# Kernel optimization log

Measured on AMD Instinct MI355X. Metric: run time of the kernel, lower is better.

## Reference

```python
import jax, jax.numpy as jnp
import numpy as np

NETWORK_STRIDE = 16
RPN_NMS_THRESHOLD = 0.7
N_OUT = 5  # top-N proposals returned ('N' in the source)
H = W = 32
NUM_ANCHORS = 9


def _conv(x, w, b, pad):
    y = jax.lax.conv_general_dilated(
        x, w, window_strides=(1, 1), padding=[(pad, pad), (pad, pad)],
        dimension_numbers=("NCHW", "OIHW", "NCHW"))
    return y + b[None, :, None, None]


def _construct_anchors(anchors_wh, h, w):
    # anchors_wh: [A,2] (already divided by NETWORK_STRIDE)
    base = jnp.concatenate([-anchors_wh / 2.0, anchors_wh / 2.0], axis=-1)  # [A,4]
    xs = jnp.arange(h, dtype=anchors_wh.dtype)
    ys = jnp.arange(w, dtype=anchors_wh.dtype)
    hf = jnp.asarray(h, anchors_wh.dtype)
    wf = jnp.asarray(w, anchors_wh.dtype)
    x1 = (base[None, None, :, 0] + xs[:, None, None]) / hf  # [h,1,A]
    y1 = (base[None, None, :, 1] + ys[None, :, None]) / wf  # [1,w,A]
    x2 = (base[None, None, :, 2] + xs[:, None, None]) / hf
    y2 = (base[None, None, :, 3] + ys[None, :, None]) / wf
    anc = jnp.stack(jnp.broadcast_arrays(x1, y1, x2, y2), axis=-1)  # [h,w,A,4]
    return anc.reshape(-1, 4)


def _deparameterize(reg, anchors):
    wa = anchors[:, 2] - anchors[:, 0]
    ha = anchors[:, 3] - anchors[:, 1]
    xa = (anchors[:, 0] + anchors[:, 2]) * 0.5
    ya = (anchors[:, 1] + anchors[:, 3]) * 0.5
    xc = reg[:, 0] * wa + xa
    yc = reg[:, 1] * ha + ya
    bw = jnp.exp(reg[:, 2]) * wa
    bh = jnp.exp(reg[:, 3]) * ha
    return jnp.stack([xc - bw / 2, yc - bh / 2, xc + bw / 2, yc + bh / 2], axis=-1)


def _pairwise_iou(a, b):
    lt = jnp.maximum(a[:, None, :2], b[None, :, :2])
    rb = jnp.minimum(a[:, None, 2:], b[None, :, 2:])
    wh = jnp.clip(rb - lt, 0.0)
    inter = wh[..., 0] * wh[..., 1]
    area_a = (a[:, 2] - a[:, 0]) * (a[:, 3] - a[:, 1])
    area_b = (b[:, 2] - b[:, 0]) * (b[:, 3] - b[:, 1])
    return inter / (area_a[:, None] + area_b[None, :] - inter)


def _nms(boxes, scores, thr):
    n = boxes.shape[0]
    order = jnp.argsort(-scores)
    boxes_s = boxes[order]
    iou = _pairwise_iou(boxes_s, boxes_s)  # [n,n], the memory-dominant intermediate
    idx = jnp.arange(n)

    def body(suppressed, i):
        keep_i = jnp.logical_not(suppressed[i])
        suppressed = suppressed | (keep_i & (iou[i] > thr) & (idx > i))
        return suppressed, keep_i

    _, kept = jax.lax.scan(body, jnp.zeros(n, dtype=bool), idx)
    # kept indices (in score order) first, padding slots pushed to the back
    sel = jnp.argsort(jnp.where(kept, idx, n))
    return order[sel]


def _forward(x, w_win, b_win, w_cls, b_cls, w_reg, b_reg, anchors_wh):
    feats = jax.nn.relu(_conv(x, w_win, b_win, 1))
    cls = _conv(feats, w_cls, b_cls, 0)
    reg = _conv(feats, w_reg, b_reg, 0)
    cls = jax.nn.softmax(cls.transpose(0, 2, 3, 1).reshape(-1, 2), axis=-1)
    reg = reg.transpose(0, 2, 3, 1).reshape(-1, 4)
    h, w = feats.shape[-2], feats.shape[-1]
    anchors = _construct_anchors(anchors_wh, h, w)
    boxes = _deparameterize(jax.lax.stop_gradient(reg), anchors)  # reg.detach()
    scores = cls[:, 0]
    keep = _nms(boxes, scores, RPN_NMS_THRESHOLD)[:N_OUT]
    return cls[keep], boxes[keep]


def setup_inputs() -> dict:
    key = jax.random.key(0)
    ks = jax.random.split(key, 4)
    anchors_px = np.array(
        [[184, 96], [128, 128], [88, 176], [368, 184], [256, 256],
         [176, 352], [736, 368], [512, 512], [352, 704]], dtype=np.float32)
    anchors_wh = jnp.asarray(anchors_px) / NETWORK_STRIDE
    x = jax.random.normal(ks[0], (1, 512, H, W), dtype=jnp.float32)
    w_win = jax.random.normal(ks[1], (512, 512, 3, 3), dtype=jnp.float32) * 0.02
    b_win = jnp.zeros((512,), jnp.float32)
    w_cls = jax.random.normal(ks[2], (2 * NUM_ANCHORS, 512, 1, 1), dtype=jnp.float32) * 0.02
    b_cls = jnp.zeros((2 * NUM_ANCHORS,), jnp.float32)
    w_reg = jax.random.normal(ks[3], (4 * NUM_ANCHORS, 512, 1, 1), dtype=jnp.float32) * 0.01
    b_reg = jnp.zeros((4 * NUM_ANCHORS,), jnp.float32)
    return {"x": x, "w_win": w_win, "b_win": b_win, "w_cls": w_cls,
            "b_cls": b_cls, "w_reg": w_reg, "b_reg": b_reg,
            "anchors_wh": anchors_wh}


def reference(x, w_win, b_win, w_cls, b_cls, w_reg, b_reg, anchors_wh):
    return _forward(x, w_win, b_win, w_cls, b_cls, w_reg, b_reg, anchors_wh)
```

## Files before the change

### kernel.cpp

```cpp
#include <hip/hip_runtime.h>
#include <math.h>


#define HH 32
#define WW 32
#define NPIX 1024
#define CIN 512
#define COUT 512
#define NA 9
#define NBOX (NPIX * NA)
#define NMS_THR 0.7f
#define NOUT 5

typedef _Float16 half8 __attribute__((ext_vector_type(8)));
typedef float f32x4 __attribute__((ext_vector_type(4)));

#define GLOAD16(src, dst) \
    __builtin_amdgcn_global_load_lds((const __attribute__((address_space(1))) void*)(src), \
                                     (__attribute__((address_space(3))) void*)(dst), 16, 0, 0)

__global__ __launch_bounds__(256) void prep_kernel(
    const float* __restrict__ x, const float* __restrict__ w,
    const float* __restrict__ w_cls, const float* __restrict__ b_cls,
    const float* __restrict__ w_reg, const float* __restrict__ b_reg,
    _Float16* __restrict__ xp_hi, _Float16* __restrict__ xp_lo,
    _Float16* __restrict__ wt_hi, _Float16* __restrict__ wt_lo,
    float* __restrict__ wt_head, float* __restrict__ bias_head)
{
    int b = blockIdx.x;
    int tid = threadIdx.x;
    if (b < 1024) {
        int t = b * 256 + tid;
#pragma unroll
        for (int q = 0; q < 9; ++q) {
            float v = w[(size_t)t * 9 + q];
            _Float16 hi = (_Float16)v;
            _Float16 lo = (_Float16)(v - (float)hi);
            wt_hi[(size_t)q * 262144 + t] = hi;
            wt_lo[(size_t)q * 262144 + t] = lo;
        }
    } else if (b < 1152) {
        __shared__ float xs[64][65];
        int bb = b - 1024;
        int ic0 = (bb & 7) * 64;
        int pix0 = (bb >> 3) * 64;
#pragma unroll
        for (int r = 0; r < 16; ++r) {
            int i = r * 4 + (tid >> 6);
            int j = tid & 63;
            xs[i][j] = x[(size_t)(ic0 + i) * NPIX + pix0 + j];
        }
        __syncthreads();
#pragma unroll
        for (int rr = 0; rr < 16; ++rr) {
            int j = rr * 4 + (tid >> 6);
            int i = tid & 63;
            float v = xs[i][j];
            int p = pix0 + j;
            int row = ((p >> 5) + 1) * 34 + (p & 31) + 1;
            _Float16 hi = (_Float16)v;
            _Float16 lo = (_Float16)(v - (float)hi);
            xp_hi[(size_t)row * 512 + ic0 + i] = hi;
            xp_lo[(size_t)row * 512 + ic0 + i] = lo;
        }
    } else if (b < 1188) {
        int base = (b - 1152) * 256 + tid;
        for (int e = base; e < 132 * 512; e += 36 * 256) {
            int br = e >> 9;
            int ic = e & 511;
            int row;
            if (br < 34) row = br;
            else if (br < 68) row = 33 * 34 + (br - 34);
            else { int c2 = br - 68; row = (1 + (c2 >> 1)) * 34 + (c2 & 1) * 33; }
            xp_hi[(size_t)row * 512 + ic] = (_Float16)0.f;
            xp_lo[(size_t)row * 512 + ic] = (_Float16)0.f;
        }
    } else {
        int t = (b - 1188) * 256 + tid;
        int o = t & 63;
        int ic0 = (t >> 6) * 16;
#pragma unroll
        for (int k = 0; k < 16; ++k) {
            int ic = ic0 + k;
            float v = 0.f;
            if (o < 18)      v = w_cls[(size_t)o * CIN + ic];
            else if (o < 54) v = w_reg[(size_t)(o - 18) * CIN + ic];
            wt_head[(size_t)ic * 64 + o] = v;
        }
        if (t < 64) {
            float bv = 0.f;
            if (t < 18)      bv = b_cls[t];
            else if (t < 54) bv = b_reg[t - 18];
            bias_head[t] = bv;
        }
    }
}

#define BUFSZ 24576
__global__ __launch_bounds__(128) void conv_gemm_kernel(
    const _Float16* __restrict__ xp_hi, const _Float16* __restrict__ xp_lo,
    const _Float16* __restrict__ wt_hi, const _Float16* __restrict__ wt_lo,
    float* __restrict__ part)
{
    __shared__ __align__(16) char smem[2 * BUFSZ];
    int bid = blockIdx.x;
    int xcd = bid & 7, rest = bid >> 3;
    int nt = (xcd & 3) * 2 + (rest & 1);
    int ks = xcd >> 2;
    int mt = rest >> 1;
    int oc0 = nt * 64;
    int kb0 = ks * 36;

    int tid = threadIdx.x;
    int wave = tid >> 6, lane = tid & 63;

    int r8 = lane >> 3;
    int khalf = ((((lane & 7) * 16) ^ (r8 << 4)) >> 1);
    const _Float16* srcAh = xp_hi + (size_t)(mt * 34 + r8) * 512 + khalf;
    const _Float16* srcAl = xp_lo + (size_t)(mt * 34 + r8) * 512 + khalf;
    const _Float16* srcBh = wt_hi + (size_t)(oc0 + r8) * 512 + khalf;
    const _Float16* srcBl = wt_lo + (size_t)(oc0 + r8) * 512 + khalf;
    int cA0 = wave, cA1 = wave + 2;

#define STAGE(kb, bufb) do {                                                    \
        int q_ = (kb) >> 3, icc_ = (kb) & 7;                                    \
        int qy_ = (q_ * 11) >> 5; int qx_ = q_ - qy_ * 3;                       \
        size_t ao_ = (size_t)(qy_ * 34 + qx_) * 512 + icc_ * 64;                \
        size_t bo_ = (size_t)q_ * 262144 + icc_ * 64;                           \
        char* bb_ = smem + (bufb);                                              \
        GLOAD16(srcAh + ao_ + cA0 * 4096, bb_ + cA0 * 1024);                    \
        GLOAD16(srcAh + ao_ + cA1 * 4096, bb_ + cA1 * 1024);                    \
        GLOAD16(srcAl + ao_ + cA0 * 4096, bb_ + 4096 + cA0 * 1024);             \
        GLOAD16(srcAl + ao_ + cA1 * 4096, bb_ + 4096 + cA1 * 1024);             \
        GLOAD16(srcBh + bo_ + (wave) * 4096,     bb_ + 8192  + (wave) * 1024);  \
        GLOAD16(srcBh + bo_ + (wave + 2) * 4096, bb_ + 8192  + (wave + 2) * 1024); \
        GLOAD16(srcBh + bo_ + (wave + 4) * 4096, bb_ + 8192  + (wave + 4) * 1024); \
        GLOAD16(srcBh + bo_ + (wave + 6) * 4096, bb_ + 8192  + (wave + 6) * 1024); \
        GLOAD16(srcBl + bo_ + (wave) * 4096,     bb_ + 16384 + (wave) * 1024);  \
        GLOAD16(srcBl + bo_ + (wave + 2) * 4096, bb_ + 16384 + (wave + 2) * 1024); \
        GLOAD16(srcBl + bo_ + (wave + 4) * 4096, bb_ + 16384 + (wave + 4) * 1024); \
        GLOAD16(srcBl + bo_ + (wave + 6) * 4096, bb_ + 16384 + (wave + 6) * 1024); \
    } while (0)

    int wn = wave;
    int ml = lane & 15, kq = lane >> 4;
    int swz = (ml & 7) << 4;
    int aoff = ml * 128 + ((kq * 16) ^ swz);
    int boff = (wn * 32 + ml) * 128 + ((kq * 16) ^ swz);

    f32x4 hh[2][2], co[2][2];
#pragma unroll
    for (int m = 0; m < 2; ++m)
#pragma unroll
        for (int n = 0; n < 2; ++n) { hh[m][n] = (f32x4)0.f; co[m][n] = (f32x4)0.f; }

#define MF(a, b, c) __builtin_amdgcn_mfma_f32_16x16x32_f16(a, b, c, 0, 0, 0)
#define COMPUTE(bufb) do {                                                      \
        const char* bb_ = smem + (bufb);                                        \
        _Pragma("unroll")                                                       \
        for (int s2 = 0; s2 < 2; ++s2) {                                        \
            int kx_ = s2 * 64;                                                  \
            half8 ah0 = *(const half8*)(bb_ + (aoff ^ kx_));                    \
            half8 ah1 = *(const half8*)(bb_ + 2048  + (aoff ^ kx_));            \
            half8 al0 = *(const half8*)(bb_ + 4096  + (aoff ^ kx_));            \
            half8 al1 = *(const half8*)(bb_ + 6144  + (aoff ^ kx_));            \
            half8 bh0 = *(const half8*)(bb_ + 8192  + (boff ^ kx_));            \
            half8 bh1 = *(const half8*)(bb_ + 10240 + (boff ^ kx_));            \
            half8 bl0 = *(const half8*)(bb_ + 16384 + (boff ^ kx_));            \
            half8 bl1 = *(const half8*)(bb_ + 18432 + (boff ^ kx_));            \
            hh[0][0] = MF(ah0, bh0, hh[0][0]);                                  \
            hh[0][1] = MF(ah0, bh1, hh[0][1]);                                  \
            hh[1][0] = MF(ah1, bh0, hh[1][0]);                                  \
            hh[1][1] = MF(ah1, bh1, hh[1][1]);                                  \
            co[0][0] = MF(ah0, bl0, co[0][0]); co[0][0] = MF(al0, bh0, co[0][0]); \
            co[0][1] = MF(ah0, bl1, co[0][1]); co[0][1] = MF(al0, bh1, co[0][1]); \
            co[1][0] = MF(ah1, bl0, co[1][0]); co[1][0] = MF(al1, bh0, co[1][0]); \
            co[1][1] = MF(ah1, bl1, co[1][1]); co[1][1] = MF(al1, bh1, co[1][1]); \
        }                                                                       \
    } while (0)

    STAGE(kb0, 0);
    __syncthreads();
    int buf = 0;
    for (int i = 0; i < 36; ++i) {
        if (i < 35) STAGE(kb0 + i + 1, (buf ^ 1) * BUFSZ);
        COMPUTE(buf * BUFSZ);
        __syncthreads();
        buf ^= 1;
    }

    float* outp = part + (size_t)ks * 524288;
#pragma unroll
    for (int m = 0; m < 2; ++m)
#pragma unroll
        for (int n = 0; n < 2; ++n) {
            int oc = oc0 + wn * 32 + n * 16 + ml;
#pragma unroll
            for (int j = 0; j < 4; ++j) {
                int pixc = m * 16 + kq * 4 + j;
                outp[(size_t)(mt * 32 + pixc) * 512 + oc] = hh[m][n][j] + co[m][n][j];
            }
        }
#undef STAGE
#undef COMPUTE
#undef MF
}

__global__ __launch_bounds__(64) void head_kernel(
    const float* __restrict__ part, const float* __restrict__ b_win,
    const float* __restrict__ wt_head, const float* __restrict__ bias_head,
    const float* __restrict__ anchors_wh,
    float* __restrict__ boxes, float* __restrict__ probs)
{
    int p = blockIdx.x;
    int lane = threadIdx.x;

    __shared__ float fs[CIN];
    __shared__ float dots[64];

    const float4* p0 = (const float4*)(part + (size_t)p * 512);
    const float4* p1 = (const float4*)(part + 524288 + (size_t)p * 512);
    const float4* bw = (const float4*)b_win;
    float4* fs4 = (float4*)fs;
#pragma unroll
    for (int i = 0; i < 2; ++i) {
        int j = i * 64 + lane;
        float4 a = p0[j], b = p1[j], c = bw[j];
        float4 r;
        r.x = fmaxf(a.x + b.x + c.x, 0.f);
        r.y = fmaxf(a.y + b.y + c.y, 0.f);
        r.z = fmaxf(a.z + b.z + c.z, 0.f);
        r.w = fmaxf(a.w + b.w + c.w, 0.f);
        fs4[j] = r;
    }
    __syncthreads();

    {
        const float* wcol = wt_head + lane;
        float a0 = 0.f, a1 = 0.f, a2 = 0.f, a3 = 0.f;
#pragma unroll 8
        for (int ic = 0; ic < CIN; ic += 4) {
            a0 = fmaf(fs[ic + 0], wcol[(ic + 0) * 64], a0);
            a1 = fmaf(fs[ic + 1], wcol[(ic + 1) * 64], a1);
            a2 = fmaf(fs[ic + 2], wcol[(ic + 2) * 64], a2);
            a3 = fmaf(fs[ic + 3], wcol[(ic + 3) * 64], a3);
        }
        dots[lane] = ((a0 + a1) + (a2 + a3)) + bias_head[lane];
    }
    __syncthreads();

    if (lane < NA) {
        int a = lane;
        float c0 = dots[2 * a], c1 = dots[2 * a + 1];
        float m = fmaxf(c0, c1);
        float e0 = expf(c0 - m), e1 = expf(c1 - m);
        float inv = 1.f / (e0 + e1);
        float p0s = e0 * inv, p1s = e1 * inv;

        int ih = p >> 5, iw = p & 31;
        float wa = anchors_wh[2 * a + 0];
        float ha = anchors_wh[2 * a + 1];
        float fih = (float)ih, fiw = (float)iw;
        float ax1 = (-(wa / 2.0f) + fih) / 32.0f;
        float ay1 = (-(ha / 2.0f) + fiw) / 32.0f;
        float ax2 = ((wa / 2.0f) + fih) / 32.0f;
        float ay2 = ((ha / 2.0f) + fiw) / 32.0f;
        float wab = ax2 - ax1;
        float hab = ay2 - ay1;
        float xa = (ax1 + ax2) * 0.5f;
        float ya = (ay1 + ay2) * 0.5f;

        float rg0 = dots[18 + 4 * a + 0];
        float rg1 = dots[18 + 4 * a + 1];
        float rg2 = dots[18 + 4 * a + 2];
        float rg3 = dots[18 + 4 * a + 3];
        float xc = rg0 * wab + xa;
        float yc = rg1 * hab + ya;
        float bw2 = expf(rg2) * wab;
        float bh2 = expf(rg3) * hab;

        int idx = p * NA + a;
        float4 bx;
        bx.x = xc - bw2 / 2.0f;
        bx.y = yc - bh2 / 2.0f;
        bx.z = xc + bw2 / 2.0f;
        bx.w = yc + bh2 / 2.0f;
        ((float4*)boxes)[idx] = bx;
        probs[idx * 2 + 0] = p0s;
        probs[idx * 2 + 1] = p1s;
    }
}

__global__ __launch_bounds__(1024) void nms_kernel(
    const float* __restrict__ boxes, const float* __restrict__ probs,
    float* __restrict__ out)
{
    __shared__ float redv[16];
    __shared__ int   redi[16];
    __shared__ int   keep[NOUT];
    __shared__ float bbox[4];

    int tid = threadIdx.x;
    float4 myb[9];
    float  mys[9];
#pragma unroll
    for (int j = 0; j < 9; ++j) {
        int i = j * 1024 + tid;
        myb[j] = ((const float4*)boxes)[i];
        mys[j] = probs[2 * i];
    }

    for (int k = 0; k < NOUT; ++k) {
        float bv = -1e30f;
        int   bi = NBOX;
#pragma unroll
        for (int j = 0; j < 9; ++j) {
            int idx = j * 1024 + tid;
            float v = mys[j];
            if (v > bv || (v == bv && idx < bi)) { bv = v; bi = idx; }
        }
#pragma unroll
        for (int off = 32; off > 0; off >>= 1) {
            float ov = __shfl_down(bv, off);
            int   oi = __shfl_down(bi, off);
            if (ov > bv || (ov == bv && oi < bi)) { bv = ov; bi = oi; }
        }
        if ((tid & 63) == 0) { redv[tid >> 6] = bv; redi[tid >> 6] = bi; }
        __syncthreads();
        if (tid == 0) {
            float fv = redv[0]; int fi = redi[0];
#pragma unroll
            for (int w = 1; w < 16; ++w)
                if (redv[w] > fv || (redv[w] == fv && redi[w] < fi)) { fv = redv[w]; fi = redi[w]; }
            keep[k] = fi;
            float4 pb = ((const float4*)boxes)[fi];
            bbox[0] = pb.x; bbox[1] = pb.y; bbox[2] = pb.z; bbox[3] = pb.w;
        }
        __syncthreads();
        float bx0 = bbox[0], bx1 = bbox[1], bx2 = bbox[2], bx3 = bbox[3];
        float aa = (bx2 - bx0) * (bx3 - bx1);
#pragma unroll
        for (int j = 0; j < 9; ++j) {
            float4 bb = myb[j];
            float ltx = fmaxf(bx0, bb.x);
            float lty = fmaxf(bx1, bb.y);
            float rbx = fminf(bx2, bb.z);
            float rby = fminf(bx3, bb.w);
            float iw2 = fmaxf(rbx - ltx, 0.f);
            float ih2 = fmaxf(rby - lty, 0.f);
            float inter = iw2 * ih2;
            float ab = (bb.z - bb.x) * (bb.w - bb.y);
            float iou = inter / (aa + ab - inter);
            if (iou > NMS_THR) mys[j] = -1e30f;
        }
    }

    if (tid < NOUT) {
        int ki = keep[tid];
        out[tid * 2 + 0] = probs[(size_t)ki * 2 + 0];
        out[tid * 2 + 1] = probs[(size_t)ki * 2 + 1];
        out[2 * NOUT + tid * 4 + 0] = boxes[(size_t)ki * 4 + 0];
        out[2 * NOUT + tid * 4 + 1] = boxes[(size_t)ki * 4 + 1];
        out[2 * NOUT + tid * 4 + 2] = boxes[(size_t)ki * 4 + 2];
        out[2 * NOUT + tid * 4 + 3] = boxes[(size_t)ki * 4 + 3];
    }
}

extern "C" void kernel_launch(void* const* d_in, const int* in_sizes, int n_in,
                              void* d_out, int out_size, void* d_ws, size_t ws_size,
                              hipStream_t stream)
{
    const float* x          = (const float*)d_in[0];
    const float* w_win      = (const float*)d_in[1];
    const float* b_win      = (const float*)d_in[2];
    const float* w_cls      = (const float*)d_in[3];
    const float* b_cls      = (const float*)d_in[4];
    const float* w_reg      = (const float*)d_in[5];
    const float* b_reg      = (const float*)d_in[6];
    const float* anchors_wh = (const float*)d_in[7];

    char* wsb = (char*)d_ws;
    float*     part      = (float*)(wsb);
    float*     boxes     = (float*)(wsb + 4194304);
    float*     probs     = (float*)(wsb + 4341760);
    _Float16*  xp_hi     = (_Float16*)(wsb + 4415488);
    _Float16*  xp_lo     = (_Float16*)(wsb + 5599232);
    _Float16*  wt_hi     = (_Float16*)(wsb + 6782976);
    _Float16*  wt_lo     = (_Float16*)(wsb + 11501568);
    float*     wt_head   = (float*)(wsb + 16220160);
    float*     bias_head = (float*)(wsb + 16351232);

    prep_kernel<<<1196, 256, 0, stream>>>(x, w_win, w_cls, b_cls, w_reg, b_reg,
                                          xp_hi, xp_lo, wt_hi, wt_lo,
                                          wt_head, bias_head);
    conv_gemm_kernel<<<512, 128, 0, stream>>>(xp_hi, xp_lo, wt_hi, wt_lo, part);
    head_kernel<<<NPIX, 64, 0, stream>>>(part, b_win, wt_head, bias_head,
                                         anchors_wh, boxes, probs);
    nms_kernel<<<1, 1024, 0, stream>>>(boxes, probs, (float*)d_out);
}
```

Baseline: 140.0 us.

## Restructure conv GEMM to stage input halo once and split-K by channels

Result: faster. 133.4 us (-4.7%).

```diff
diff --git a/kernel.cpp b/kernel.cpp
--- a/kernel.cpp
+++ b/kernel.cpp
@@ -96,113 +96,116 @@
     }
 }
 
-#define BUFSZ 24576
-__global__ __launch_bounds__(128) void conv_gemm_kernel(
+#define A_LO 30720
+#define B0_B 61440
+#define B1_B 94208
+#define BXOR (B0_B ^ B1_B)
+
+__global__ __launch_bounds__(256) void conv_gemm_kernel(
     const _Float16* __restrict__ xp_hi, const _Float16* __restrict__ xp_lo,
     const _Float16* __restrict__ wt_hi, const _Float16* __restrict__ wt_lo,
     float* __restrict__ part)
 {
-    __shared__ __align__(16) char smem[2 * BUFSZ];
+    __shared__ __align__(16) char smem[126976];
+
     int bid = blockIdx.x;
-    int xcd = bid & 7, rest = bid >> 3;
-    int nt = (xcd & 3) * 2 + (rest & 1);
-    int ks = xcd >> 2;
-    int mt = rest >> 1;
-    int oc0 = nt * 64;
-    int kb0 = ks * 36;
+    int c   = bid & 31;
+    int mtb = bid >> 5;
+    int nt2 = c >> 3;
+    int ks  = c & 7;
+    int oc0 = nt2 * 128;
+    int icc = ks * 64;
+    int r0x = mtb * 4;
 
     int tid = threadIdx.x;
     int wave = tid >> 6, lane = tid & 63;
-
-    int r8 = lane >> 3;
-    int khalf = ((((lane & 7) * 16) ^ (r8 << 4)) >> 1);
-    const _Float16* srcAh = xp_hi + (size_t)(mt * 34 + r8) * 512 + khalf;
-    const _Float16* srcAl = xp_lo + (size_t)(mt * 34 + r8) * 512 + khalf;
-    const _Float16* srcBh = wt_hi + (size_t)(oc0 + r8) * 512 + khalf;
-    const _Float16* srcBl = wt_lo + (size_t)(oc0 + r8) * 512 + khalf;
-    int cA0 = wave, cA1 = wave + 2;
-
-#define STAGE(kb, bufb) do {                                                    \
-        int q_ = (kb) >> 3, icc_ = (kb) & 7;                                    \
-        int qy_ = (q_ * 11) >> 5; int qx_ = q_ - qy_ * 3;                       \
-        size_t ao_ = (size_t)(qy_ * 34 + qx_) * 512 + icc_ * 64;                \
-        size_t bo_ = (size_t)q_ * 262144 + icc_ * 64;                           \
-        char* bb_ = smem + (bufb);                                              \
-        GLOAD16(srcAh + ao_ + cA0 * 4096, bb_ + cA0 * 1024);                    \
-        GLOAD16(srcAh + ao_ + cA1 * 4096, bb_ + cA1 * 1024);                    \
-        GLOAD16(srcAl + ao_ + cA0 * 4096, bb_ + 4096 + cA0 * 1024);             \
-        GLOAD16(srcAl + ao_ + cA1 * 4096, bb_ + 4096 + cA1 * 1024);             \
-        GLOAD16(srcBh + bo_ + (wave) * 4096,     bb_ + 8192  + (wave) * 1024);  \
-        GLOAD16(srcBh + bo_ + (wave + 2) * 4096, bb_ + 8192  + (wave + 2) * 1024); \
-        GLOAD16(srcBh + bo_ + (wave + 4) * 4096, bb_ + 8192  + (wave + 4) * 1024); \
-        GLOAD16(srcBh + bo_ + (wave + 6) * 4096, bb_ + 8192  + (wave + 6) * 1024); \
-        GLOAD16(srcBl + bo_ + (wave) * 4096,     bb_ + 16384 + (wave) * 1024);  \
-        GLOAD16(srcBl + bo_ + (wave + 2) * 4096, bb_ + 16384 + (wave + 2) * 1024); \
-        GLOAD16(srcBl + bo_ + (wave + 4) * 4096, bb_ + 16384 + (wave + 4) * 1024); \
-        GLOAD16(srcBl + bo_ + (wave + 6) * 4096, bb_ + 16384 + (wave + 6) * 1024); \
-    } while (0)
-
-    int wn = wave;
+    int l3 = lane >> 3;
+    int khalf = ((((lane & 7) * 16) ^ (l3 << 4)) >> 1);
+    const _Float16* sAh = xp_hi + (size_t)l3 * 512 + khalf;
+    const _Float16* sAl = xp_lo + (size_t)l3 * 512 + khalf;
+    const _Float16* sBh = wt_hi + (size_t)l3 * 512 + khalf;
+    const _Float16* sBl = wt_lo + (size_t)l3 * 512 + khalf;
+
+    for (int g = wave; g < 30; g += 4) {
+        int row = g / 5, pg = g - row * 5;
+        size_t so = ((size_t)(r0x + row) * 34 + pg * 8) * 512 + icc;
+        int dd = (row * 40 + pg * 8) * 128;
+        GLOAD16(sAh + so, smem + dd);
+        GLOAD16(sAl + so, smem + A_LO + dd);
+    }
+#define STAGEB(q_, bbase) do {                                                 \
+        size_t bo_ = (size_t)(q_) * 262144 + (size_t)oc0 * 512 + icc;          \
+        for (int og = wave; og < 16; og += 4) {                                \
+            size_t so_ = bo_ + (size_t)og * 8 * 512;                           \
+            GLOAD16(sBh + so_, smem + (bbase) + og * 1024);                    \
+            GLOAD16(sBl + so_, smem + (bbase) + 16384 + og * 1024);            \
+        } } while (0)
+    STAGEB(0, B0_B);
+    __syncthreads();
+
+    int wm = wave >> 1, wn = wave & 1;
     int ml = lane & 15, kq = lane >> 4;
-    int swz = (ml & 7) << 4;
-    int aoff = ml * 128 + ((kq * 16) ^ swz);
-    int boff = (wn * 32 + ml) * 128 + ((kq * 16) ^ swz);
-
-    f32x4 hh[2][2], co[2][2];
-#pragma unroll
-    for (int m = 0; m < 2; ++m)
-#pragma unroll
-        for (int n = 0; n < 2; ++n) { hh[m][n] = (f32x4)0.f; co[m][n] = (f32x4)0.f; }
-
-#define MF(a, b, c) __builtin_amdgcn_mfma_f32_16x16x32_f16(a, b, c, 0, 0, 0)
-#define COMPUTE(bufb) do {                                                      \
-        const char* bb_ = smem + (bufb);                                        \
-        _Pragma("unroll")                                                       \
-        for (int s2 = 0; s2 < 2; ++s2) {                                        \
-            int kx_ = s2 * 64;                                                  \
-            half8 ah0 = *(const half8*)(bb_ + (aoff ^ kx_));                    \
-            half8 ah1 = *(const half8*)(bb_ + 2048  + (aoff ^ kx_));            \
-            half8 al0 = *(const half8*)(bb_ + 4096  + (aoff ^ kx_));            \
-            half8 al1 = *(const half8*)(bb_ + 6144  + (aoff ^ kx_));            \
-            half8 bh0 = *(const half8*)(bb_ + 8192  + (boff ^ kx_));            \
-            half8 bh1 = *(const half8*)(bb_ + 10240 + (boff ^ kx_));            \
-            half8 bl0 = *(const half8*)(bb_ + 16384 + (boff ^ kx_));            \
-            half8 bl1 = *(const half8*)(bb_ + 18432 + (boff ^ kx_));            \
-            hh[0][0] = MF(ah0, bh0, hh[0][0]);                                  \
-            hh[0][1] = MF(ah0, bh1, hh[0][1]);                                  \
-            hh[1][0] = MF(ah1, bh0, hh[1][0]);                                  \
-            hh[1][1] = MF(ah1, bh1, hh[1][1]);                                  \
-            co[0][0] = MF(ah0, bl0, co[0][0]); co[0][0] = MF(al0, bh0, co[0][0]); \
-            co[0][1] = MF(ah0, bl1, co[0][1]); co[0][1] = MF(al0, bh1, co[0][1]); \
-            co[1][0] = MF(ah1, bl0, co[1][0]); co[1][0] = MF(al1, bh0, co[1][0]); \
-            co[1][1] = MF(ah1, bl1, co[1][1]); co[1][1] = MF(al1, bh1, co[1][1]); \
-        }                                                                       \
-    } while (0)
-
-    STAGE(kb0, 0);
-    __syncthreads();
-    int buf = 0;
-    for (int i = 0; i < 36; ++i) {
-        if (i < 35) STAGE(kb0 + i + 1, (buf ^ 1) * BUFSZ);
-        COMPUTE(buf * BUFSZ);
+
+    f32x4 hh[4][4], co[4][4];
+#pragma unroll
+    for (int m = 0; m < 4; ++m)
+#pragma unroll
+        for (int n = 0; n < 4; ++n) { hh[m][n] = (f32x4)0.f; co[m][n] = (f32x4)0.f; }
+
+#define MF(a, b, cc) __builtin_amdgcn_mfma_f32_16x16x32_f16(a, b, cc, 0, 0, 0)
+
+    int bb = B0_B;
+#pragma unroll 1
+    for (int q = 0; q < 9; ++q) {
+        int qy = (q * 11) >> 5;
+        int qx = q - qy * 3;
+        if (q < 8) STAGEB(q + 1, bb ^ BXOR);
+
+        int pswz = ((ml + qx) & 7) << 4;
+        int bswz = (ml & 7) << 4;
+#pragma unroll
+        for (int k2 = 0; k2 < 2; ++k2) {
+            int kb = k2 * 64 + kq * 16;
+            half8 ah[4], al[4];
+#pragma unroll
+            for (int m = 0; m < 4; ++m) {
+                int row = qy + wm * 2 + (m >> 1);
+                int px  = (m & 1) * 16 + ml + qx;
+                int ao  = (row * 40 + px) * 128 + (kb ^ pswz);
+                ah[m] = *(const half8*)(smem + ao);
+                al[m] = *(const half8*)(smem + A_LO + ao);
+            }
+#pragma unroll
+            for (int n = 0; n < 4; ++n) {
+                int bo = bb + (wn * 64 + n * 16 + ml) * 128 + (kb ^ bswz);
+                half8 bh = *(const half8*)(smem + bo);
+                half8 bl = *(const half8*)(smem + 16384 + bo);
+#pragma unroll
+                for (int m = 0; m < 4; ++m) {
+                    hh[m][n] = MF(ah[m], bh, hh[m][n]);
+                    co[m][n] = MF(ah[m], bl, co[m][n]);
+                    co[m][n] = MF(al[m], bh, co[m][n]);
+                }
+            }
+        }
         __syncthreads();
-        buf ^= 1;
+        bb ^= BXOR;
     }
 
     float* outp = part + (size_t)ks * 524288;
-#pragma unroll
-    for (int m = 0; m < 2; ++m)
-#pragma unroll
-        for (int n = 0; n < 2; ++n) {
-            int oc = oc0 + wn * 32 + n * 16 + ml;
+    int pxb = mtb * 128 + wm * 64;
+#pragma unroll
+    for (int m = 0; m < 4; ++m)
+#pragma unroll
+        for (int n = 0; n < 4; ++n) {
+            int oc = oc0 + wn * 64 + n * 16 + ml;
 #pragma unroll
             for (int j = 0; j < 4; ++j) {
-                int pixc = m * 16 + kq * 4 + j;
-                outp[(size_t)(mt * 32 + pixc) * 512 + oc] = hh[m][n][j] + co[m][n][j];
+                int px = pxb + m * 16 + kq * 4 + j;
+                outp[(size_t)px * 512 + oc] = hh[m][n][j] + co[m][n][j];
             }
         }
-#undef STAGE
-#undef COMPUTE
+#undef STAGEB
 #undef MF
 }
 
@@ -218,19 +221,21 @@
     __shared__ float fs[CIN];
     __shared__ float dots[64];
 
-    const float4* p0 = (const float4*)(part + (size_t)p * 512);
-    const float4* p1 = (const float4*)(part + 524288 + (size_t)p * 512);
     const float4* bw = (const float4*)b_win;
     float4* fs4 = (float4*)fs;
 #pragma unroll
     for (int i = 0; i < 2; ++i) {
         int j = i * 64 + lane;
-        float4 a = p0[j], b = p1[j], c = bw[j];
-        float4 r;
-        r.x = fmaxf(a.x + b.x + c.x, 0.f);
-        r.y = fmaxf(a.y + b.y + c.y, 0.f);
-        r.z = fmaxf(a.z + b.z + c.z, 0.f);
-        r.w = fmaxf(a.w + b.w + c.w, 0.f);
+        float4 r = bw[j];
+#pragma unroll
+        for (int s = 0; s < 8; ++s) {
+            float4 a = ((const float4*)(part + (size_t)s * 524288 + (size_t)p * 512))[j];
+            r.x += a.x; r.y += a.y; r.z += a.z; r.w += a.w;
+        }
+        r.x = fmaxf(r.x, 0.f);
+        r.y = fmaxf(r.y, 0.f);
+        r.z = fmaxf(r.z, 0.f);
+        r.w = fmaxf(r.w, 0.f);
         fs4[j] = r;
     }
     __syncthreads();
@@ -341,15 +346,15 @@
         float aa = (bx2 - bx0) * (bx3 - bx1);
 #pragma unroll
         for (int j = 0; j < 9; ++j) {
-            float4 bb = myb[j];
-            float ltx = fmaxf(bx0, bb.x);
-            float lty = fmaxf(bx1, bb.y);
-            float rbx = fminf(bx2, bb.z);
-            float rby = fminf(bx3, bb.w);
+            float4 bbx = myb[j];
+            float ltx = fmaxf(bx0, bbx.x);
+            float lty = fmaxf(bx1, bbx.y);
+            float rbx = fminf(bx2, bbx.z);
+            float rby = fminf(bx3, bbx.w);
             float iw2 = fmaxf(rbx - ltx, 0.f);
             float ih2 = fmaxf(rby - lty, 0.f);
             float inter = iw2 * ih2;
-            float ab = (bb.z - bb.x) * (bb.w - bb.y);
+            float ab = (bbx.z - bbx.x) * (bbx.w - bbx.y);
             float iou = inter / (aa + ab - inter);
             if (iou > NMS_THR) mys[j] = -1e30f;
         }
@@ -381,19 +386,19 @@
 
     char* wsb = (char*)d_ws;
     float*     part      = (float*)(wsb);
-    float*     boxes     = (float*)(wsb + 4194304);
-    float*     probs     = (float*)(wsb + 4341760);
-    _Float16*  xp_hi     = (_Float16*)(wsb + 4415488);
-    _Float16*  xp_lo     = (_Float16*)(wsb + 5599232);
-    _Float16*  wt_hi     = (_Float16*)(wsb + 6782976);
-    _Float16*  wt_lo     = (_Float16*)(wsb + 11501568);
-    float*     wt_head   = (float*)(wsb + 16220160);
-    float*     bias_head = (float*)(wsb + 16351232);
+    float*     boxes     = (float*)(wsb + 16777216);
+    float*     probs     = (float*)(wsb + 16924672);
+    _Float16*  xp_hi     = (_Float16*)(wsb + 16998400);
+    _Float16*  xp_lo     = (_Float16*)(wsb + 18182144);
+    _Float16*  wt_hi     = (_Float16*)(wsb + 19365888);
+    _Float16*  wt_lo     = (_Float16*)(wsb + 24084480);
+    float*     wt_head   = (float*)(wsb + 28803072);
+    float*     bias_head = (float*)(wsb + 28934144);
 
     prep_kernel<<<1196, 256, 0, stream>>>(x, w_win, w_cls, b_cls, w_reg, b_reg,
                                           xp_hi, xp_lo, wt_hi, wt_lo,
                                           wt_head, bias_head);
-    conv_gemm_kernel<<<512, 128, 0, stream>>>(xp_hi, xp_lo, wt_hi, wt_lo, part);
+    conv_gemm_kernel<<<256, 256, 0, stream>>>(xp_hi, xp_lo, wt_hi, wt_lo, part);
     head_kernel<<<NPIX, 64, 0, stream>>>(part, b_win, wt_head, bias_head,
                                          anchors_wh, boxes, probs);
     nms_kernel<<<1, 1024, 0, stream>>>(boxes, probs, (float*)d_out);
```
